# Performance work log

Hardware: AMD Instinct MI355X
Metric: run time of the kernel (lower is better)

Reference implementation:

```python
import jax, jax.numpy as jnp
import numpy as np

N_NODES = 50000


def _gcn_conv(x, edge_index, W, b):
    # x: [N, F_in], edge_index: [2, E] (with self-loops already added)
    n = x.shape[0]
    src, dst = edge_index[0], edge_index[1]
    h = x @ W  # [N, F_out] transform first (as in PyG GCNConv)
    deg = jax.ops.segment_sum(jnp.ones_like(dst, dtype=h.dtype), dst, num_segments=n)
    dinv = jax.lax.rsqrt(jnp.maximum(deg, 1.0))  # self-loops guarantee deg >= 1
    norm = dinv[src] * dinv[dst]  # [E]
    msg = h[src] * norm[:, None]  # [E, F_out] gather + scale
    out = jax.ops.segment_sum(msg, dst, num_segments=n)  # scatter-add to targets
    return out + b


def setup_inputs() -> dict:
    key = jax.random.key(0)
    k1, k2, k3, k4 = jax.random.split(key, 4)
    num_features, hidden, num_classes = 128, 128, 16
    n, e = N_NODES, 800000
    x = jax.random.normal(k1, (n, num_features), dtype=jnp.float32)
    edge_index = jax.random.randint(k2, (2, e), 0, n, dtype=jnp.int64)
    # add self-loops (PyG GCNConv default add_self_loops=True)
    loops = jnp.arange(n, dtype=jnp.int64)
    edge_index = jnp.concatenate([edge_index, jnp.stack([loops, loops])], axis=1)
    s1 = 1.0 / np.sqrt(num_features)
    s2 = 1.0 / np.sqrt(hidden)
    W1 = jax.random.uniform(k3, (num_features, hidden), jnp.float32, -s1, s1)
    b1 = jnp.zeros((hidden,), jnp.float32)
    W2 = jax.random.uniform(k4, (hidden, num_classes), jnp.float32, -s2, s2)
    b2 = jnp.zeros((num_classes,), jnp.float32)
    return {"x": x, "edge_index": edge_index, "W1": W1, "b1": b1, "W2": W2, "b2": b2}


def reference(x, edge_index, W1, b1, W2, b2):
    h = jax.nn.relu(_gcn_conv(x, edge_index, W1, b1))
    # dropout is identity in eval mode (deterministic reference)
    h = _gcn_conv(h, edge_index, W2, b2)
    return jax.nn.log_softmax(h, axis=1)
```

## Files before the change

kernel.cpp:

```cpp
#include <hip/hip_runtime.h>


typedef unsigned int uint32;
typedef unsigned short ushort16;
typedef __attribute__((ext_vector_type(8))) short bf16x8;
typedef __attribute__((ext_vector_type(4))) float f32x4;

#define NBMAX 1024
#define CHUNK 4096

__device__ inline unsigned short bf16rn(float f) {
    unsigned u = __float_as_uint(f);
    return (unsigned short)((u + 0x7fffu + ((u >> 16) & 1u)) >> 16);
}

__device__ inline void bffma(float2& a, float w, uint32 u) {
    a.x = fmaf(w, __uint_as_float(u << 16), a.x);
    a.y = fmaf(w, __uint_as_float(u & 0xffff0000u), a.y);
}


__global__ __launch_bounds__(256) void k_hist(const int* __restrict__ dst,
                                              int* __restrict__ bcnt,
                                              int E, int NB) {
    __shared__ int hl[NBMAX];
    int t = threadIdx.x;
    for (int i = t; i < NB; i += 256) hl[i] = 0;
    __syncthreads();
    int stride = gridDim.x * 256;
    for (int e = blockIdx.x * 256 + t; e < E; e += stride)
        atomicAdd(&hl[dst[e] >> 8], 1);
    __syncthreads();
    for (int i = t; i < NB; i += 256)
        if (hl[i]) atomicAdd(&bcnt[i], hl[i]);
}

__global__ __launch_bounds__(1024) void k_scanB(const int* __restrict__ bcnt,
                                                int* __restrict__ bbase,
                                                int* __restrict__ bfill,
                                                int NB, int E) {
    __shared__ int s[1024];
    int t = threadIdx.x;
    int v = (t < NB) ? bcnt[t] : 0;
    s[t] = v;
    __syncthreads();
    for (int off = 1; off < 1024; off <<= 1) {
        int u = (t >= off) ? s[t - off] : 0;
        __syncthreads();
        s[t] += u;
        __syncthreads();
    }
    if (t < NB) {
        bbase[t] = s[t] - v;
        bfill[t] = 0;
    }
    if (t == 0) bbase[NB] = E;
}

__global__ __launch_bounds__(256) void k_partition(const int* __restrict__ src,
                                                   const int* __restrict__ dst,
                                                   const int* __restrict__ bbase,
                                                   int* __restrict__ bfill,
                                                   int2* __restrict__ tmp,
                                                   int E, int NB) {
    __shared__ int cntL[NBMAX];
    __shared__ int baseL[NBMAX];
    int t = threadIdx.x;
    int e0 = blockIdx.x * CHUNK;
    int e1 = min(e0 + CHUNK, E);
    for (int i = t; i < NB; i += 256) cntL[i] = 0;
    __syncthreads();
    for (int e = e0 + t; e < e1; e += 256)
        atomicAdd(&cntL[dst[e] >> 8], 1);
    __syncthreads();
    for (int i = t; i < NB; i += 256) {
        int c = cntL[i];
        baseL[i] = c ? bbase[i] + atomicAdd(&bfill[i], c) : 0;
        cntL[i] = 0;
    }
    __syncthreads();
    for (int e = e0 + t; e < e1; e += 256) {
        int s = src[e], d = dst[e];
        int b = d >> 8;
        int r = atomicAdd(&cntL[b], 1);
        tmp[baseL[b] + r] = make_int2(s, d);
    }
}

__global__ __launch_bounds__(256) void k_bsort(const int2* __restrict__ tmp,
                                               const int* __restrict__ bbase,
                                               int* __restrict__ ssrc,
                                               int* __restrict__ rs,
                                               float* __restrict__ dinv,
                                               int N) {
    __shared__ int cnt[256];
    __shared__ int ofs[256];
    int t = threadIdx.x;
    int b = blockIdx.x;
    int base = bbase[b];
    int endb = bbase[b + 1];
    int node0 = b << 8;

    cnt[t] = 0;
    __syncthreads();
    for (int i = base + t; i < endb; i += 256)
        atomicAdd(&cnt[tmp[i].y & 255], 1);
    __syncthreads();

    int v = cnt[t];
    __syncthreads();
    for (int off = 1; off < 256; off <<= 1) {
        int u = (t >= off) ? cnt[t - off] : 0;
        __syncthreads();
        cnt[t] += u;
        __syncthreads();
    }
    int node = node0 + t;
    if (node < N) {
        dinv[node] = rsqrtf(fmaxf((float)v, 1.0f));
        rs[node] = base + cnt[t];
    }
    ofs[t] = base + cnt[t] - v;
    __syncthreads();

    for (int i = base + t; i < endb; i += 256) {
        int2 rec = tmp[i];
        int pos = atomicAdd(&ofs[rec.y & 255], 1);
        ssrc[pos] = rec.x;
    }
}


__global__ __launch_bounds__(256) void k_gemm1(const float* __restrict__ x,
                                               const float* __restrict__ W,
                                               ushort16* __restrict__ h, int N) {
    __shared__ unsigned short Wl[128 * 136];
    int t = threadIdx.x;
    const float4* Wg4 = (const float4*)W;
    for (int g = t; g < 128 * 32; g += 256) {
        int k = g >> 5, n4 = (g & 31) * 4;
        float4 v = Wg4[g];
        Wl[(n4 + 0) * 136 + k] = bf16rn(v.x);
        Wl[(n4 + 1) * 136 + k] = bf16rn(v.y);
        Wl[(n4 + 2) * 136 + k] = bf16rn(v.z);
        Wl[(n4 + 3) * 136 + k] = bf16rn(v.w);
    }
    __syncthreads();

    int wave = t >> 6, lane = t & 63;
    int quad = lane >> 4, ln = lane & 15;
    int rowbase = blockIdx.x * 64 + wave * 16;
    int arow = rowbase + ln;
    int rclamp = min(arow, N - 1);

    f32x4 acc[8];
    #pragma unroll
    for (int ct = 0; ct < 8; ++ct) acc[ct] = (f32x4){0.f, 0.f, 0.f, 0.f};

    #pragma unroll
    for (int q = 0; q < 4; ++q) {
        const float4* xr = (const float4*)(x + (size_t)rclamp * 128 + q * 32 + quad * 8);
        float4 a0 = xr[0], a1 = xr[1];
        bf16x8 afr;
        afr[0] = (short)bf16rn(a0.x); afr[1] = (short)bf16rn(a0.y);
        afr[2] = (short)bf16rn(a0.z); afr[3] = (short)bf16rn(a0.w);
        afr[4] = (short)bf16rn(a1.x); afr[5] = (short)bf16rn(a1.y);
        afr[6] = (short)bf16rn(a1.z); afr[7] = (short)bf16rn(a1.w);
        #pragma unroll
        for (int ct = 0; ct < 8; ++ct) {
            bf16x8 bfr = *(const bf16x8*)&Wl[(ct * 16 + ln) * 136 + q * 32 + quad * 8];
            acc[ct] = __builtin_amdgcn_mfma_f32_16x16x32_bf16(afr, bfr, acc[ct], 0, 0, 0);
        }
    }

    #pragma unroll
    for (int i = 0; i < 4; ++i) {
        int r = rowbase + quad * 4 + i;
        if (r < N) {
            ushort16* hp = h + (size_t)r * 128 + ln;
            #pragma unroll
            for (int ct = 0; ct < 8; ++ct)
                hp[ct * 16] = bf16rn(acc[ct][i]);
        }
    }
}

__global__ __launch_bounds__(256) void k_pull1(const int* __restrict__ rs,
                                               const int* __restrict__ ssrc,
                                               const float* __restrict__ dinv,
                                               const uint32* __restrict__ h,
                                               uint32* __restrict__ out1, int N) {
    int n = (blockIdx.x * 256 + threadIdx.x) >> 6;
    if (n >= N) return;
    int lane = threadIdx.x & 63;
    int start = __builtin_amdgcn_readfirstlane((n == 0) ? 0 : rs[n - 1]);
    int end   = __builtin_amdgcn_readfirstlane(rs[n]);
    float dn = dinv[n];
    float2 a0 = {0.f, 0.f}, a1 = {0.f, 0.f}, a2 = {0.f, 0.f}, a3 = {0.f, 0.f};
    int j = start;
    for (; j + 3 < end; j += 4) {
        int s0 = __builtin_amdgcn_readfirstlane(ssrc[j]);
        int s1 = __builtin_amdgcn_readfirstlane(ssrc[j + 1]);
        int s2 = __builtin_amdgcn_readfirstlane(ssrc[j + 2]);
        int s3 = __builtin_amdgcn_readfirstlane(ssrc[j + 3]);
        uint32 u0 = h[(size_t)s0 * 64 + lane];
        uint32 u1 = h[(size_t)s1 * 64 + lane];
        uint32 u2 = h[(size_t)s2 * 64 + lane];
        uint32 u3 = h[(size_t)s3 * 64 + lane];
        float w0 = dn * dinv[s0];
        float w1 = dn * dinv[s1];
        float w2 = dn * dinv[s2];
        float w3 = dn * dinv[s3];
        bffma(a0, w0, u0);
        bffma(a1, w1, u1);
        bffma(a2, w2, u2);
        bffma(a3, w3, u3);
    }
    for (; j < end; ++j) {
        int s0 = __builtin_amdgcn_readfirstlane(ssrc[j]);
        uint32 u0 = h[(size_t)s0 * 64 + lane];
        bffma(a0, dn * dinv[s0], u0);
    }
    float rx = (a0.x + a1.x) + (a2.x + a3.x);
    float ry = (a0.y + a1.y) + (a2.y + a3.y);
    out1[(size_t)n * 64 + lane] = ((uint32)bf16rn(ry) << 16) | bf16rn(rx);
}

__global__ __launch_bounds__(256) void k_gemm2(const uint32* __restrict__ out1,
                                               const float* __restrict__ b1,
                                               const float* __restrict__ W2,
                                               ushort16* __restrict__ h2, int N) {
    __shared__ float W2T[16 * 132];
    __shared__ float b1l[128];
    __shared__ float al[32 * 132];
    int t = threadIdx.x;
    int row0 = blockIdx.x * 32;

    for (int g = t; g < 2048; g += 256) {
        int k = g >> 4, f = g & 15;
        W2T[f * 132 + k] = W2[g];
    }
    if (t < 128) b1l[t] = b1[t];
    __syncthreads();

    float4* al4 = (float4*)al;
    const uint4* o4 = (const uint4*)out1;
    for (int g = t; g < 32 * 16; g += 256) {
        int r = g >> 4, k8 = g & 15;
        uint4 u = {0u, 0u, 0u, 0u};
        if (row0 + r < N) u = o4[(size_t)(row0 + r) * 16 + k8];
        const float* bb = &b1l[k8 * 8];
        float4 v0, v1;
        v0.x = fmaxf(__uint_as_float(u.x << 16)          + bb[0], 0.f);
        v0.y = fmaxf(__uint_as_float(u.x & 0xffff0000u)  + bb[1], 0.f);
        v0.z = fmaxf(__uint_as_float(u.y << 16)          + bb[2], 0.f);
        v0.w = fmaxf(__uint_as_float(u.y & 0xffff0000u)  + bb[3], 0.f);
        v1.x = fmaxf(__uint_as_float(u.z << 16)          + bb[4], 0.f);
        v1.y = fmaxf(__uint_as_float(u.z & 0xffff0000u)  + bb[5], 0.f);
        v1.z = fmaxf(__uint_as_float(u.w << 16)          + bb[6], 0.f);
        v1.w = fmaxf(__uint_as_float(u.w & 0xffff0000u)  + bb[7], 0.f);
        al4[r * 33 + k8 * 2]     = v0;
        al4[r * 33 + k8 * 2 + 1] = v1;
    }
    __syncthreads();

    int f = t & 15, r0 = t >> 4;
    const float4* W4 = (const float4*)W2T;
    float acc0 = 0.f, acc1 = 0.f;
    #pragma unroll 8
    for (int k4 = 0; k4 < 32; ++k4) {
        float4 w  = W4[f * 33 + k4];
        float4 x0 = al4[r0 * 33 + k4];
        float4 x1 = al4[(r0 + 16) * 33 + k4];
        acc0 = fmaf(x0.x, w.x, acc0); acc0 = fmaf(x0.y, w.y, acc0);
        acc0 = fmaf(x0.z, w.z, acc0); acc0 = fmaf(x0.w, w.w, acc0);
        acc1 = fmaf(x1.x, w.x, acc1); acc1 = fmaf(x1.y, w.y, acc1);
        acc1 = fmaf(x1.z, w.z, acc1); acc1 = fmaf(x1.w, w.w, acc1);
    }
    if (row0 + r0 < N)      h2[(size_t)(row0 + r0) * 16 + f] = bf16rn(acc0);
    if (row0 + r0 + 16 < N) h2[(size_t)(row0 + r0 + 16) * 16 + f] = bf16rn(acc1);
}

__global__ __launch_bounds__(256) void k_pull2(const int* __restrict__ rs,
                                               const int* __restrict__ ssrc,
                                               const float* __restrict__ dinv,
                                               const uint32* __restrict__ h2,
                                               const float* __restrict__ b2,
                                               float* __restrict__ out, int N) {
    int idx = blockIdx.x * 256 + threadIdx.x;
    int n = idx >> 3;
    if (n >= N) return;
    int c = idx & 7;
    int start = (n == 0) ? 0 : rs[n - 1];
    int end = rs[n];
    float dn = dinv[n];
    float acc0 = 0.f, acc1 = 0.f;
    for (int j = start; j < end; ++j) {
        int s = ssrc[j];
        float w = dn * dinv[s];
        uint32 u = h2[(size_t)s * 8 + c];
        acc0 = fmaf(w, __uint_as_float(u << 16), acc0);
        acc1 = fmaf(w, __uint_as_float(u & 0xffff0000u), acc1);
    }
    float v0 = acc0 + b2[2 * c];
    float v1 = acc1 + b2[2 * c + 1];
    float m = fmaxf(v0, v1);
    #pragma unroll
    for (int off = 1; off < 8; off <<= 1) m = fmaxf(m, __shfl_xor(m, off));
    float s = expf(v0 - m) + expf(v1 - m);
    #pragma unroll
    for (int off = 1; off < 8; off <<= 1) s += __shfl_xor(s, off);
    float ls = logf(s);
    float2 r = {v0 - m - ls, v1 - m - ls};
    ((float2*)out)[(size_t)n * 8 + c] = r;
}

extern "C" void kernel_launch(void* const* d_in, const int* in_sizes, int n_in,
                              void* d_out, int out_size, void* d_ws, size_t ws_size,
                              hipStream_t stream) {
    const float* x  = (const float*)d_in[0];
    const int*   ei = (const int*)d_in[1];
    const float* W1 = (const float*)d_in[2];
    const float* b1 = (const float*)d_in[3];
    const float* W2 = (const float*)d_in[4];
    const float* b2 = (const float*)d_in[5];
    float* out = (float*)d_out;

    const int E = in_sizes[1] / 2;
    const int N = in_sizes[0] / 128;
    const int NB = (N + 255) >> 8;
    const int* src  = ei;
    const int* dstv = ei + E;

    const int Npad = (N + 255) & ~255;
    const int Epad = (E + 255) & ~255;
    int*   bcnt  = (int*)d_ws;
    int*   bbase = bcnt + NBMAX;
    int*   bfill = bbase + NBMAX + 256;
    int*   rs    = bfill + NBMAX;
    float* dinv  = (float*)(rs + Npad);
    int2*  tmp   = (int2*)(dinv + Npad);
    int*   ssrc  = (int*)(tmp + Epad);
    ushort16* h  = (ushort16*)(ssrc + Epad);
    uint32* out1 = (uint32*)(h + (size_t)N * 128);
    ushort16* h2 = (ushort16*)h;

    hipMemsetAsync(bcnt, 0, NBMAX * sizeof(int), stream);
    k_hist<<<512, 256, 0, stream>>>(dstv, bcnt, E, NB);
    k_scanB<<<1, 1024, 0, stream>>>(bcnt, bbase, bfill, NB, E);
    k_partition<<<(E + CHUNK - 1) / CHUNK, 256, 0, stream>>>(src, dstv, bbase,
                                                             bfill, tmp, E, NB);
    k_bsort<<<NB, 256, 0, stream>>>(tmp, bbase, ssrc, rs, dinv, N);

    k_gemm1<<<(N + 63) / 64, 256, 0, stream>>>(x, W1, h, N);

    k_pull1<<<(N * 64 + 255) / 256, 256, 0, stream>>>(rs, ssrc, dinv,
                                                      (const uint32*)h, out1, N);

    k_gemm2<<<(N + 31) / 32, 256, 0, stream>>>(out1, b1, W2, h2, N);

    k_pull2<<<(N * 8 + 255) / 256, 256, 0, stream>>>(rs, ssrc, dinv,
                                                     (const uint32*)h2, b2, out, N);
}
```

Measured before the change: 202.8 us.

## Fuse all GCN stages into one cooperative persistent kernel with grid syncs

Merges histogram, scan, partition, bucket sort, both GEMMs and both aggregation passes into a single persistent kernel. The stages are separated by cooperative grid.sync calls, with a fallback that runs one phase per launch. The goal is to remove launch overhead and the memset between the nine launches. In exchange it risks lower occupancy with a capped grid, grid-sync cost, and idle blocks in the single-block scan phase. It also overlaps the sort-to-GEMM1 boundary with no sync, splits GEMM1 into two W halves to fit shared memory, and unrolls the pull1 loop to 8.

```diff
diff --git a/kernel.cpp b/kernel.cpp
--- a/kernel.cpp
+++ b/kernel.cpp
@@ -1,17 +1,21 @@
 #include <hip/hip_runtime.h>
+#include <hip/hip_cooperative_groups.h>
+
+namespace cg = cooperative_groups;
 
 
 typedef unsigned int uint32;
-typedef unsigned short ushort16;
+typedef unsigned short u16;
 typedef __attribute__((ext_vector_type(8))) short bf16x8;
 typedef __attribute__((ext_vector_type(4))) float f32x4;
 
 #define NBMAX 1024
 #define CHUNK 4096
-
-__device__ inline unsigned short bf16rn(float f) {
+#define SMEM_BYTES 25856
+
+__device__ inline u16 bf16rn(float f) {
     unsigned u = __float_as_uint(f);
-    return (unsigned short)((u + 0x7fffu + ((u >> 16) & 1u)) >> 16);
+    return (u16)((u + 0x7fffu + ((u >> 16) & 1u)) >> 16);
 }
 
 __device__ inline void bffma(float2& a, float w, uint32 u) {
@@ -19,300 +23,324 @@
     a.y = fmaf(w, __uint_as_float(u & 0xffff0000u), a.y);
 }
 
-
-__global__ __launch_bounds__(256) void k_hist(const int* __restrict__ dst,
-                                              int* __restrict__ bcnt,
-                                              int E, int NB) {
-    __shared__ int hl[NBMAX];
-    int t = threadIdx.x;
-    for (int i = t; i < NB; i += 256) hl[i] = 0;
-    __syncthreads();
-    int stride = gridDim.x * 256;
-    for (int e = blockIdx.x * 256 + t; e < E; e += stride)
-        atomicAdd(&hl[dst[e] >> 8], 1);
-    __syncthreads();
-    for (int i = t; i < NB; i += 256)
-        if (hl[i]) atomicAdd(&bcnt[i], hl[i]);
-}
-
-__global__ __launch_bounds__(1024) void k_scanB(const int* __restrict__ bcnt,
-                                                int* __restrict__ bbase,
-                                                int* __restrict__ bfill,
-                                                int NB, int E) {
-    __shared__ int s[1024];
-    int t = threadIdx.x;
-    int v = (t < NB) ? bcnt[t] : 0;
-    s[t] = v;
-    __syncthreads();
-    for (int off = 1; off < 1024; off <<= 1) {
-        int u = (t >= off) ? s[t - off] : 0;
-        __syncthreads();
-        s[t] += u;
-        __syncthreads();
-    }
-    if (t < NB) {
-        bbase[t] = s[t] - v;
-        bfill[t] = 0;
-    }
-    if (t == 0) bbase[NB] = E;
-}
-
-__global__ __launch_bounds__(256) void k_partition(const int* __restrict__ src,
-                                                   const int* __restrict__ dst,
-                                                   const int* __restrict__ bbase,
-                                                   int* __restrict__ bfill,
-                                                   int2* __restrict__ tmp,
-                                                   int E, int NB) {
-    __shared__ int cntL[NBMAX];
-    __shared__ int baseL[NBMAX];
-    int t = threadIdx.x;
-    int e0 = blockIdx.x * CHUNK;
-    int e1 = min(e0 + CHUNK, E);
-    for (int i = t; i < NB; i += 256) cntL[i] = 0;
-    __syncthreads();
-    for (int e = e0 + t; e < e1; e += 256)
-        atomicAdd(&cntL[dst[e] >> 8], 1);
-    __syncthreads();
-    for (int i = t; i < NB; i += 256) {
-        int c = cntL[i];
-        baseL[i] = c ? bbase[i] + atomicAdd(&bfill[i], c) : 0;
-        cntL[i] = 0;
-    }
-    __syncthreads();
-    for (int e = e0 + t; e < e1; e += 256) {
-        int s = src[e], d = dst[e];
-        int b = d >> 8;
-        int r = atomicAdd(&cntL[b], 1);
-        tmp[baseL[b] + r] = make_int2(s, d);
-    }
-}
-
-__global__ __launch_bounds__(256) void k_bsort(const int2* __restrict__ tmp,
-                                               const int* __restrict__ bbase,
-                                               int* __restrict__ ssrc,
-                                               int* __restrict__ rs,
-                                               float* __restrict__ dinv,
-                                               int N) {
-    __shared__ int cnt[256];
-    __shared__ int ofs[256];
-    int t = threadIdx.x;
-    int b = blockIdx.x;
-    int base = bbase[b];
-    int endb = bbase[b + 1];
-    int node0 = b << 8;
-
-    cnt[t] = 0;
-    __syncthreads();
-    for (int i = base + t; i < endb; i += 256)
-        atomicAdd(&cnt[tmp[i].y & 255], 1);
-    __syncthreads();
-
-    int v = cnt[t];
-    __syncthreads();
-    for (int off = 1; off < 256; off <<= 1) {
-        int u = (t >= off) ? cnt[t - off] : 0;
-        __syncthreads();
-        cnt[t] += u;
-        __syncthreads();
-    }
-    int node = node0 + t;
-    if (node < N) {
-        dinv[node] = rsqrtf(fmaxf((float)v, 1.0f));
-        rs[node] = base + cnt[t];
-    }
-    ofs[t] = base + cnt[t] - v;
-    __syncthreads();
-
-    for (int i = base + t; i < endb; i += 256) {
-        int2 rec = tmp[i];
-        int pos = atomicAdd(&ofs[rec.y & 255], 1);
-        ssrc[pos] = rec.x;
-    }
-}
-
-
-__global__ __launch_bounds__(256) void k_gemm1(const float* __restrict__ x,
-                                               const float* __restrict__ W,
-                                               ushort16* __restrict__ h, int N) {
-    __shared__ unsigned short Wl[128 * 136];
-    int t = threadIdx.x;
-    const float4* Wg4 = (const float4*)W;
-    for (int g = t; g < 128 * 32; g += 256) {
-        int k = g >> 5, n4 = (g & 31) * 4;
-        float4 v = Wg4[g];
-        Wl[(n4 + 0) * 136 + k] = bf16rn(v.x);
-        Wl[(n4 + 1) * 136 + k] = bf16rn(v.y);
-        Wl[(n4 + 2) * 136 + k] = bf16rn(v.z);
-        Wl[(n4 + 3) * 136 + k] = bf16rn(v.w);
-    }
-    __syncthreads();
-
-    int wave = t >> 6, lane = t & 63;
-    int quad = lane >> 4, ln = lane & 15;
-    int rowbase = blockIdx.x * 64 + wave * 16;
-    int arow = rowbase + ln;
-    int rclamp = min(arow, N - 1);
-
-    f32x4 acc[8];
-    #pragma unroll
-    for (int ct = 0; ct < 8; ++ct) acc[ct] = (f32x4){0.f, 0.f, 0.f, 0.f};
-
-    #pragma unroll
-    for (int q = 0; q < 4; ++q) {
-        const float4* xr = (const float4*)(x + (size_t)rclamp * 128 + q * 32 + quad * 8);
-        float4 a0 = xr[0], a1 = xr[1];
-        bf16x8 afr;
-        afr[0] = (short)bf16rn(a0.x); afr[1] = (short)bf16rn(a0.y);
-        afr[2] = (short)bf16rn(a0.z); afr[3] = (short)bf16rn(a0.w);
-        afr[4] = (short)bf16rn(a1.x); afr[5] = (short)bf16rn(a1.y);
-        afr[6] = (short)bf16rn(a1.z); afr[7] = (short)bf16rn(a1.w);
+__global__ __launch_bounds__(256, 2) void k_mega(
+    const float* __restrict__ x, const int* __restrict__ src,
+    const int* __restrict__ dstv,
+    const float* __restrict__ W1, const float* __restrict__ b1,
+    const float* __restrict__ W2, const float* __restrict__ b2,
+    int* __restrict__ bcnt, int* __restrict__ bbase, int* __restrict__ bfill,
+    int* __restrict__ rs, float* __restrict__ dinv,
+    int2* __restrict__ tmp, int* __restrict__ ssrc,
+    u16* __restrict__ h, uint32* __restrict__ out1,
+    float* __restrict__ outp, int N, int E, int NB, int p0, int p1)
+{
+    __shared__ __align__(16) unsigned char smem[SMEM_BYTES];
+    const int t = threadIdx.x;
+    const int nbk = gridDim.x;
+    const int gtid = blockIdx.x * 256 + t;
+    const int gsz = nbk * 256;
+
+    cg::grid_group grid = cg::this_grid();
+    #define INPH(p) (p0 <= (p) && (p) <= p1)
+    #define GSYNC(p) if (p0 < (p) && (p) <= p1) grid.sync()
+
+    if (INPH(0)) {
+        for (int i = gtid; i < NBMAX; i += gsz) bcnt[i] = 0;
+    }
+    GSYNC(1);
+
+    if (INPH(1)) {
+        int* hl = (int*)smem;
+        for (int i = t; i < NB; i += 256) hl[i] = 0;
+        __syncthreads();
+        for (int e = gtid; e < E; e += gsz) atomicAdd(&hl[dstv[e] >> 8], 1);
+        __syncthreads();
+        for (int i = t; i < NB; i += 256)
+            if (hl[i]) atomicAdd(&bcnt[i], hl[i]);
+        __syncthreads();
+    }
+    GSYNC(2);
+
+    if (INPH(2) && blockIdx.x == 0) {
+        int* s = (int*)smem;
+        int v[4];
+        int sum = 0;
         #pragma unroll
-        for (int ct = 0; ct < 8; ++ct) {
-            bf16x8 bfr = *(const bf16x8*)&Wl[(ct * 16 + ln) * 136 + q * 32 + quad * 8];
-            acc[ct] = __builtin_amdgcn_mfma_f32_16x16x32_bf16(afr, bfr, acc[ct], 0, 0, 0);
-        }
-    }
-
-    #pragma unroll
-    for (int i = 0; i < 4; ++i) {
-        int r = rowbase + quad * 4 + i;
-        if (r < N) {
-            ushort16* hp = h + (size_t)r * 128 + ln;
+        for (int i = 0; i < 4; ++i) {
+            int idx = t * 4 + i;
+            v[i] = (idx < NB) ? bcnt[idx] : 0;
+            sum += v[i];
+        }
+        s[t] = sum;
+        __syncthreads();
+        for (int off = 1; off < 256; off <<= 1) {
+            int u = (t >= off) ? s[t - off] : 0;
+            __syncthreads();
+            s[t] += u;
+            __syncthreads();
+        }
+        int excl = (t > 0) ? s[t - 1] : 0;
+        #pragma unroll
+        for (int i = 0; i < 4; ++i) {
+            int idx = t * 4 + i;
+            if (idx < NB) { bbase[idx] = excl; bfill[idx] = 0; }
+            excl += v[i];
+        }
+        if (t == 0) bbase[NB] = E;
+        __syncthreads();
+    }
+    GSYNC(3);
+
+    if (INPH(3)) {
+        int* cntL = (int*)smem;
+        int* baseL = cntL + NBMAX;
+        int nchunk = (E + CHUNK - 1) / CHUNK;
+        for (int c = blockIdx.x; c < nchunk; c += nbk) {
+            int e0 = c * CHUNK, e1 = min(e0 + CHUNK, E);
+            for (int i = t; i < NB; i += 256) cntL[i] = 0;
+            __syncthreads();
+            for (int e = e0 + t; e < e1; e += 256)
+                atomicAdd(&cntL[dstv[e] >> 8], 1);
+            __syncthreads();
+            for (int i = t; i < NB; i += 256) {
+                int cc = cntL[i];
+                baseL[i] = cc ? bbase[i] + atomicAdd(&bfill[i], cc) : 0;
+                cntL[i] = 0;
+            }
+            __syncthreads();
+            for (int e = e0 + t; e < e1; e += 256) {
+                int sv = src[e], d = dstv[e];
+                int b = d >> 8;
+                int r = atomicAdd(&cntL[b], 1);
+                tmp[baseL[b] + r] = make_int2(sv, d);
+            }
+            __syncthreads();
+        }
+    }
+    GSYNC(4);
+
+    if (INPH(4)) {
+        int* cnt = (int*)smem;
+        int* ofs = cnt + 256;
+        for (int b = blockIdx.x; b < NB; b += nbk) {
+            int base = bbase[b];
+            int endb = bbase[b + 1];
+            int node0 = b << 8;
+            cnt[t] = 0;
+            __syncthreads();
+            for (int i = base + t; i < endb; i += 256)
+                atomicAdd(&cnt[tmp[i].y & 255], 1);
+            __syncthreads();
+            int v = cnt[t];
+            __syncthreads();
+            for (int off = 1; off < 256; off <<= 1) {
+                int u = (t >= off) ? cnt[t - off] : 0;
+                __syncthreads();
+                cnt[t] += u;
+                __syncthreads();
+            }
+            int node = node0 + t;
+            if (node < N) {
+                dinv[node] = rsqrtf(fmaxf((float)v, 1.0f));
+                rs[node] = base + cnt[t];
+            }
+            ofs[t] = base + cnt[t] - v;
+            __syncthreads();
+            for (int i = base + t; i < endb; i += 256) {
+                int2 rec = tmp[i];
+                int pos = atomicAdd(&ofs[rec.y & 255], 1);
+                ssrc[pos] = rec.x;
+            }
+            __syncthreads();
+        }
+    }
+
+    if (INPH(5)) {
+        u16* Wl = (u16*)smem;
+        int wave = t >> 6, lane = t & 63;
+        int quad = lane >> 4, ln = lane & 15;
+        int ntile = (N + 63) / 64;
+        const float4* Wg4 = (const float4*)W1;
+        for (int half = 0; half < 2; ++half) {
+            __syncthreads();
+            for (int g = t; g < 64 * 32; g += 256) {
+                int k = g >> 4, nq = g & 15;
+                float4 v = Wg4[k * 32 + half * 16 + nq];
+                int n4 = nq * 4;
+                Wl[(n4 + 0) * 136 + k] = bf16rn(v.x);
+                Wl[(n4 + 1) * 136 + k] = bf16rn(v.y);
+                Wl[(n4 + 2) * 136 + k] = bf16rn(v.z);
+                Wl[(n4 + 3) * 136 + k] = bf16rn(v.w);
+            }
+            __syncthreads();
+            for (int tile = blockIdx.x; tile < ntile; tile += nbk) {
+                int rowbase = tile * 64 + wave * 16;
+                int rclamp = min(rowbase + ln, N - 1);
+                f32x4 acc[4];
+                #pragma unroll
+                for (int ct = 0; ct < 4; ++ct) acc[ct] = (f32x4){0.f, 0.f, 0.f, 0.f};
+                #pragma unroll
+                for (int q = 0; q < 4; ++q) {
+                    const float4* xr =
+                        (const float4*)(x + (size_t)rclamp * 128 + q * 32 + quad * 8);
+                    float4 a0 = xr[0], a1 = xr[1];
+                    bf16x8 afr;
+                    afr[0] = (short)bf16rn(a0.x); afr[1] = (short)bf16rn(a0.y);
+                    afr[2] = (short)bf16rn(a0.z); afr[3] = (short)bf16rn(a0.w);
+                    afr[4] = (short)bf16rn(a1.x); afr[5] = (short)bf16rn(a1.y);
+                    afr[6] = (short)bf16rn(a1.z); afr[7] = (short)bf16rn(a1.w);
+                    #pragma unroll
+                    for (int ct = 0; ct < 4; ++ct) {
+                        bf16x8 bfr =
+                            *(const bf16x8*)&Wl[(ct * 16 + ln) * 136 + q * 32 + quad * 8];
+                        acc[ct] = __builtin_amdgcn_mfma_f32_16x16x32_bf16(
+                            afr, bfr, acc[ct], 0, 0, 0);
+                    }
+                }
+                #pragma unroll
+                for (int i = 0; i < 4; ++i) {
+                    int r = rowbase + quad * 4 + i;
+                    if (r < N) {
+                        u16* hp = h + (size_t)r * 128 + half * 64 + ln;
+                        #pragma unroll
+                        for (int ct = 0; ct < 4; ++ct)
+                            hp[ct * 16] = bf16rn(acc[ct][i]);
+                    }
+                }
+            }
+        }
+    }
+    GSYNC(6);
+
+    if (INPH(6)) {
+        int wave = t >> 6, lane = t & 63;
+        const uint32* hu = (const uint32*)h;
+        int ngrp = (N + 3) >> 2;
+        for (int g = blockIdx.x; g < ngrp; g += nbk) {
+            int n = g * 4 + wave;
+            if (n >= N) continue;
+            int start = __builtin_amdgcn_readfirstlane((n == 0) ? 0 : rs[n - 1]);
+            int end   = __builtin_amdgcn_readfirstlane(rs[n]);
+            float dn = dinv[n];
+            float2 a[8];
             #pragma unroll
-            for (int ct = 0; ct < 8; ++ct)
-                hp[ct * 16] = bf16rn(acc[ct][i]);
-        }
-    }
-}
-
-__global__ __launch_bounds__(256) void k_pull1(const int* __restrict__ rs,
-                                               const int* __restrict__ ssrc,
-                                               const float* __restrict__ dinv,
-                                               const uint32* __restrict__ h,
-                                               uint32* __restrict__ out1, int N) {
-    int n = (blockIdx.x * 256 + threadIdx.x) >> 6;
-    if (n >= N) return;
-    int lane = threadIdx.x & 63;
-    int start = __builtin_amdgcn_readfirstlane((n == 0) ? 0 : rs[n - 1]);
-    int end   = __builtin_amdgcn_readfirstlane(rs[n]);
-    float dn = dinv[n];
-    float2 a0 = {0.f, 0.f}, a1 = {0.f, 0.f}, a2 = {0.f, 0.f}, a3 = {0.f, 0.f};
-    int j = start;
-    for (; j + 3 < end; j += 4) {
-        int s0 = __builtin_amdgcn_readfirstlane(ssrc[j]);
-        int s1 = __builtin_amdgcn_readfirstlane(ssrc[j + 1]);
-        int s2 = __builtin_amdgcn_readfirstlane(ssrc[j + 2]);
-        int s3 = __builtin_amdgcn_readfirstlane(ssrc[j + 3]);
-        uint32 u0 = h[(size_t)s0 * 64 + lane];
-        uint32 u1 = h[(size_t)s1 * 64 + lane];
-        uint32 u2 = h[(size_t)s2 * 64 + lane];
-        uint32 u3 = h[(size_t)s3 * 64 + lane];
-        float w0 = dn * dinv[s0];
-        float w1 = dn * dinv[s1];
-        float w2 = dn * dinv[s2];
-        float w3 = dn * dinv[s3];
-        bffma(a0, w0, u0);
-        bffma(a1, w1, u1);
-        bffma(a2, w2, u2);
-        bffma(a3, w3, u3);
-    }
-    for (; j < end; ++j) {
-        int s0 = __builtin_amdgcn_readfirstlane(ssrc[j]);
-        uint32 u0 = h[(size_t)s0 * 64 + lane];
-        bffma(a0, dn * dinv[s0], u0);
-    }
-    float rx = (a0.x + a1.x) + (a2.x + a3.x);
-    float ry = (a0.y + a1.y) + (a2.y + a3.y);
-    out1[(size_t)n * 64 + lane] = ((uint32)bf16rn(ry) << 16) | bf16rn(rx);
-}
-
-__global__ __launch_bounds__(256) void k_gemm2(const uint32* __restrict__ out1,
-                                               const float* __restrict__ b1,
-                                               const float* __restrict__ W2,
-                                               ushort16* __restrict__ h2, int N) {
-    __shared__ float W2T[16 * 132];
-    __shared__ float b1l[128];
-    __shared__ float al[32 * 132];
-    int t = threadIdx.x;
-    int row0 = blockIdx.x * 32;
-
-    for (int g = t; g < 2048; g += 256) {
-        int k = g >> 4, f = g & 15;
-        W2T[f * 132 + k] = W2[g];
-    }
-    if (t < 128) b1l[t] = b1[t];
-    __syncthreads();
-
-    float4* al4 = (float4*)al;
-    const uint4* o4 = (const uint4*)out1;
-    for (int g = t; g < 32 * 16; g += 256) {
-        int r = g >> 4, k8 = g & 15;
-        uint4 u = {0u, 0u, 0u, 0u};
-        if (row0 + r < N) u = o4[(size_t)(row0 + r) * 16 + k8];
-        const float* bb = &b1l[k8 * 8];
-        float4 v0, v1;
-        v0.x = fmaxf(__uint_as_float(u.x << 16)          + bb[0], 0.f);
-        v0.y = fmaxf(__uint_as_float(u.x & 0xffff0000u)  + bb[1], 0.f);
-        v0.z = fmaxf(__uint_as_float(u.y << 16)          + bb[2], 0.f);
-        v0.w = fmaxf(__uint_as_float(u.y & 0xffff0000u)  + bb[3], 0.f);
-        v1.x = fmaxf(__uint_as_float(u.z << 16)          + bb[4], 0.f);
-        v1.y = fmaxf(__uint_as_float(u.z & 0xffff0000u)  + bb[5], 0.f);
-        v1.z = fmaxf(__uint_as_float(u.w << 16)          + bb[6], 0.f);
-        v1.w = fmaxf(__uint_as_float(u.w & 0xffff0000u)  + bb[7], 0.f);
-        al4[r * 33 + k8 * 2]     = v0;
-        al4[r * 33 + k8 * 2 + 1] = v1;
-    }
-    __syncthreads();
-
-    int f = t & 15, r0 = t >> 4;
-    const float4* W4 = (const float4*)W2T;
-    float acc0 = 0.f, acc1 = 0.f;
-    #pragma unroll 8
-    for (int k4 = 0; k4 < 32; ++k4) {
-        float4 w  = W4[f * 33 + k4];
-        float4 x0 = al4[r0 * 33 + k4];
-        float4 x1 = al4[(r0 + 16) * 33 + k4];
-        acc0 = fmaf(x0.x, w.x, acc0); acc0 = fmaf(x0.y, w.y, acc0);
-        acc0 = fmaf(x0.z, w.z, acc0); acc0 = fmaf(x0.w, w.w, acc0);
-        acc1 = fmaf(x1.x, w.x, acc1); acc1 = fmaf(x1.y, w.y, acc1);
-        acc1 = fmaf(x1.z, w.z, acc1); acc1 = fmaf(x1.w, w.w, acc1);
-    }
-    if (row0 + r0 < N)      h2[(size_t)(row0 + r0) * 16 + f] = bf16rn(acc0);
-    if (row0 + r0 + 16 < N) h2[(size_t)(row0 + r0 + 16) * 16 + f] = bf16rn(acc1);
-}
-
-__global__ __launch_bounds__(256) void k_pull2(const int* __restrict__ rs,
-                                               const int* __restrict__ ssrc,
-                                               const float* __restrict__ dinv,
-                                               const uint32* __restrict__ h2,
-                                               const float* __restrict__ b2,
-                                               float* __restrict__ out, int N) {
-    int idx = blockIdx.x * 256 + threadIdx.x;
-    int n = idx >> 3;
-    if (n >= N) return;
-    int c = idx & 7;
-    int start = (n == 0) ? 0 : rs[n - 1];
-    int end = rs[n];
-    float dn = dinv[n];
-    float acc0 = 0.f, acc1 = 0.f;
-    for (int j = start; j < end; ++j) {
-        int s = ssrc[j];
-        float w = dn * dinv[s];
-        uint32 u = h2[(size_t)s * 8 + c];
-        acc0 = fmaf(w, __uint_as_float(u << 16), acc0);
-        acc1 = fmaf(w, __uint_as_float(u & 0xffff0000u), acc1);
-    }
-    float v0 = acc0 + b2[2 * c];
-    float v1 = acc1 + b2[2 * c + 1];
-    float m = fmaxf(v0, v1);
-    #pragma unroll
-    for (int off = 1; off < 8; off <<= 1) m = fmaxf(m, __shfl_xor(m, off));
-    float s = expf(v0 - m) + expf(v1 - m);
-    #pragma unroll
-    for (int off = 1; off < 8; off <<= 1) s += __shfl_xor(s, off);
-    float ls = logf(s);
-    float2 r = {v0 - m - ls, v1 - m - ls};
-    ((float2*)out)[(size_t)n * 8 + c] = r;
+            for (int i = 0; i < 8; ++i) a[i] = (float2){0.f, 0.f};
+            int j = start;
+            for (; j + 7 < end; j += 8) {
+                int si[8];
+                uint32 u[8];
+                float w[8];
+                #pragma unroll
+                for (int i = 0; i < 8; ++i)
+                    si[i] = __builtin_amdgcn_readfirstlane(ssrc[j + i]);
+                #pragma unroll
+                for (int i = 0; i < 8; ++i)
+                    u[i] = hu[(size_t)si[i] * 64 + lane];
+                #pragma unroll
+                for (int i = 0; i < 8; ++i)
+                    w[i] = dn * dinv[si[i]];
+                #pragma unroll
+                for (int i = 0; i < 8; ++i)
+                    bffma(a[i], w[i], u[i]);
+            }
+            for (; j < end; ++j) {
+                int s0 = __builtin_amdgcn_readfirstlane(ssrc[j]);
+                bffma(a[0], dn * dinv[s0], hu[(size_t)s0 * 64 + lane]);
+            }
+            float rx = ((a[0].x + a[1].x) + (a[2].x + a[3].x)) +
+                       ((a[4].x + a[5].x) + (a[6].x + a[7].x));
+            float ry = ((a[0].y + a[1].y) + (a[2].y + a[3].y)) +
+                       ((a[4].y + a[5].y) + (a[6].y + a[7].y));
+            out1[(size_t)n * 64 + lane] = ((uint32)bf16rn(ry) << 16) | bf16rn(rx);
+        }
+    }
+    GSYNC(7);
+
+    if (INPH(7)) {
+        float* W2T = (float*)smem;
+        float* b1l = W2T + 16 * 132;
+        float4* al4 = (float4*)(b1l + 128);
+        u16* h2 = h;
+        for (int g = t; g < 2048; g += 256) {
+            int k = g >> 4, f = g & 15;
+            W2T[f * 132 + k] = W2[g];
+        }
+        if (t < 128) b1l[t] = b1[t];
+        __syncthreads();
+
+        int f = t & 15, r0 = t >> 4;
+        const float4* W4 = (const float4*)W2T;
+        const uint4* o4 = (const uint4*)out1;
+        int ntile = (N + 31) / 32;
+        for (int tile = blockIdx.x; tile < ntile; tile += nbk) {
+            int row0 = tile * 32;
+            for (int g = t; g < 32 * 16; g += 256) {
+                int r = g >> 4, k8 = g & 15;
+                uint4 u = {0u, 0u, 0u, 0u};
+                if (row0 + r < N) u = o4[(size_t)(row0 + r) * 16 + k8];
+                const float* bb = &b1l[k8 * 8];
+                float4 v0, v1;
+                v0.x = fmaxf(__uint_as_float(u.x << 16)         + bb[0], 0.f);
+                v0.y = fmaxf(__uint_as_float(u.x & 0xffff0000u) + bb[1], 0.f);
+                v0.z = fmaxf(__uint_as_float(u.y << 16)         + bb[2], 0.f);
+                v0.w = fmaxf(__uint_as_float(u.y & 0xffff0000u) + bb[3], 0.f);
+                v1.x = fmaxf(__uint_as_float(u.z << 16)         + bb[4], 0.f);
+                v1.y = fmaxf(__uint_as_float(u.z & 0xffff0000u) + bb[5], 0.f);
+                v1.z = fmaxf(__uint_as_float(u.w << 16)         + bb[6], 0.f);
+                v1.w = fmaxf(__uint_as_float(u.w & 0xffff0000u) + bb[7], 0.f);
+                al4[r * 33 + k8 * 2]     = v0;
+                al4[r * 33 + k8 * 2 + 1] = v1;
+            }
+            __syncthreads();
+            float acc0 = 0.f, acc1 = 0.f;
+            #pragma unroll 8
+            for (int k4 = 0; k4 < 32; ++k4) {
+                float4 w  = W4[f * 33 + k4];
+                float4 x0 = al4[r0 * 33 + k4];
+                float4 x1 = al4[(r0 + 16) * 33 + k4];
+                acc0 = fmaf(x0.x, w.x, acc0); acc0 = fmaf(x0.y, w.y, acc0);
+                acc0 = fmaf(x0.z, w.z, acc0); acc0 = fmaf(x0.w, w.w, acc0);
+                acc1 = fmaf(x1.x, w.x, acc1); acc1 = fmaf(x1.y, w.y, acc1);
+                acc1 = fmaf(x1.z, w.z, acc1); acc1 = fmaf(x1.w, w.w, acc1);
+            }
+            if (row0 + r0 < N)      h2[(size_t)(row0 + r0) * 16 + f] = bf16rn(acc0);
+            if (row0 + r0 + 16 < N) h2[(size_t)(row0 + r0 + 16) * 16 + f] = bf16rn(acc1);
+            __syncthreads();
+        }
+    }
+    GSYNC(8);
+
+    if (INPH(8)) {
+        const uint32* h2u = (const uint32*)h;
+        for (int idx = gtid; idx < N * 8; idx += gsz) {
+            int n = idx >> 3;
+            int c = idx & 7;
+            int start = (n == 0) ? 0 : rs[n - 1];
+            int end = rs[n];
+            float dn = dinv[n];
+            float acc0 = 0.f, acc1 = 0.f;
+            for (int j = start; j < end; ++j) {
+                int s = ssrc[j];
+                float w = dn * dinv[s];
+                uint32 u = h2u[(size_t)s * 8 + c];
+                acc0 = fmaf(w, __uint_as_float(u << 16), acc0);
+                acc1 = fmaf(w, __uint_as_float(u & 0xffff0000u), acc1);
+            }
+            float v0 = acc0 + b2[2 * c];
+            float v1 = acc1 + b2[2 * c + 1];
+            float m = fmaxf(v0, v1);
+            #pragma unroll
+            for (int off = 1; off < 8; off <<= 1) m = fmaxf(m, __shfl_xor(m, off));
+            float s = expf(v0 - m) + expf(v1 - m);
+            #pragma unroll
+            for (int off = 1; off < 8; off <<= 1) s += __shfl_xor(s, off);
+            float ls = logf(s);
+            float2 r = {v0 - m - ls, v1 - m - ls};
+            ((float2*)outp)[(size_t)n * 8 + c] = r;
+        }
+    }
+    #undef INPH
+    #undef GSYNC
 }
 
 extern "C" void kernel_launch(void* const* d_in, const int* in_sizes, int n_in,
@@ -324,7 +352,7 @@
     const float* b1 = (const float*)d_in[3];
     const float* W2 = (const float*)d_in[4];
     const float* b2 = (const float*)d_in[5];
-    float* out = (float*)d_out;
+    float* outp = (float*)d_out;
 
     const int E = in_sizes[1] / 2;
     const int N = in_sizes[0] / 128;
@@ -341,24 +369,46 @@
     float* dinv  = (float*)(rs + Npad);
     int2*  tmp   = (int2*)(dinv + Npad);
     int*   ssrc  = (int*)(tmp + Epad);
-    ushort16* h  = (ushort16*)(ssrc + Epad);
+    u16*   h     = (u16*)(ssrc + Epad);
     uint32* out1 = (uint32*)(h + (size_t)N * 128);
-    ushort16* h2 = (ushort16*)h;
-
-    hipMemsetAsync(bcnt, 0, NBMAX * sizeof(int), stream);
-    k_hist<<<512, 256, 0, stream>>>(dstv, bcnt, E, NB);
-    k_scanB<<<1, 1024, 0, stream>>>(bcnt, bbase, bfill, NB, E);
-    k_partition<<<(E + CHUNK - 1) / CHUNK, 256, 0, stream>>>(src, dstv, bbase,
-                                                             bfill, tmp, E, NB);
-    k_bsort<<<NB, 256, 0, stream>>>(tmp, bbase, ssrc, rs, dinv, N);
-
-    k_gemm1<<<(N + 63) / 64, 256, 0, stream>>>(x, W1, h, N);
-
-    k_pull1<<<(N * 64 + 255) / 256, 256, 0, stream>>>(rs, ssrc, dinv,
-                                                      (const uint32*)h, out1, N);
-
-    k_gemm2<<<(N + 31) / 32, 256, 0, stream>>>(out1, b1, W2, h2, N);
-
-    k_pull2<<<(N * 8 + 255) / 256, 256, 0, stream>>>(rs, ssrc, dinv,
-                                                     (const uint32*)h2, b2, out, N);
+
+    int dev = 0;
+    hipGetDevice(&dev);
+    int coop = 0;
+    hipDeviceGetAttribute(&coop, hipDeviceAttributeCooperativeLaunch, dev);
+    int numCU = 0;
+    hipDeviceGetAttribute(&numCU, hipDeviceAttributeMultiprocessorCount, dev);
+    int maxB = 0;
+    hipOccupancyMaxActiveBlocksPerMultiprocessor(&maxB, k_mega, 256, 0);
+
+    if (coop && maxB >= 1 && numCU >= 1) {
+        int gridB = maxB * numCU;
+        if (gridB > 2048) gridB = 2048;
+        int p0 = 0, p1 = 8;
+        void* args[] = {
+            (void*)&x, (void*)&src, (void*)&dstv,
+            (void*)&W1, (void*)&b1, (void*)&W2, (void*)&b2,
+            (void*)&bcnt, (void*)&bbase, (void*)&bfill,
+            (void*)&rs, (void*)&dinv, (void*)&tmp, (void*)&ssrc,
+            (void*)&h, (void*)&out1, (void*)&outp,
+            (void*)&N, (void*)&E, (void*)&NB, (void*)&p0, (void*)&p1,
+        };
+        hipLaunchCooperativeKernel((const void*)k_mega, dim3(gridB), dim3(256),
+                                   args, 0, stream);
+    } else {
+        const int nchunk = (E + CHUNK - 1) / CHUNK;
+        #define LP(ph, g) k_mega<<<(g), 256, 0, stream>>>( \
+            x, src, dstv, W1, b1, W2, b2, bcnt, bbase, bfill, rs, dinv, tmp, \
+            ssrc, h, out1, outp, N, E, NB, (ph), (ph))
+        LP(0, 64);
+        LP(1, 512);
+        LP(2, 1);
+        LP(3, nchunk);
+        LP(4, NB);
+        LP(5, (N + 63) / 64);
+        LP(6, (N + 3) / 4);
+        LP(7, (N + 31) / 32);
+        LP(8, (N * 8 + 255) / 256);
+        #undef LP
+    }
 }
```

Result: slower. 535.6 us (+164.1%).

## Fuse destination histogram into GEMM1 launch and deepen pull1 gather unroll

Applied to the files above, without the earlier changes.

Merges the dst-bucket histogram and the first GEMM into one launch, with extra blocks doing the histogram into per-block partial arrays instead of global atomics. This removes the memset and a separate launch and lets the histogram overlap with the MFMA work. k_scanB now sums the partials itself. The layer-1 pull loop is unrolled from 4 to 8 edges with 8 accumulators to keep more gathers in flight, at the cost of more registers. The partials buffer holds 128 blocks, which caps E at about 1M edges.

```diff
diff --git a/kernel.cpp b/kernel.cpp
--- a/kernel.cpp
+++ b/kernel.cpp
@@ -2,16 +2,17 @@
 
 
 typedef unsigned int uint32;
-typedef unsigned short ushort16;
+typedef unsigned short u16;
 typedef __attribute__((ext_vector_type(8))) short bf16x8;
 typedef __attribute__((ext_vector_type(4))) float f32x4;
 
 #define NBMAX 1024
 #define CHUNK 4096
-
-__device__ inline unsigned short bf16rn(float f) {
+#define EH 8192
+
+__device__ inline u16 bf16rn(float f) {
     unsigned u = __float_as_uint(f);
-    return (unsigned short)((u + 0x7fffu + ((u >> 16) & 1u)) >> 16);
+    return (u16)((u + 0x7fffu + ((u >> 16) & 1u)) >> 16);
 }
 
 __device__ inline void bffma(float2& a, float w, uint32 u) {
@@ -19,124 +20,30 @@
     a.y = fmaf(w, __uint_as_float(u & 0xffff0000u), a.y);
 }
 
-
-__global__ __launch_bounds__(256) void k_hist(const int* __restrict__ dst,
-                                              int* __restrict__ bcnt,
-                                              int E, int NB) {
-    __shared__ int hl[NBMAX];
-    int t = threadIdx.x;
-    for (int i = t; i < NB; i += 256) hl[i] = 0;
-    __syncthreads();
-    int stride = gridDim.x * 256;
-    for (int e = blockIdx.x * 256 + t; e < E; e += stride)
-        atomicAdd(&hl[dst[e] >> 8], 1);
-    __syncthreads();
-    for (int i = t; i < NB; i += 256)
-        if (hl[i]) atomicAdd(&bcnt[i], hl[i]);
-}
-
-__global__ __launch_bounds__(1024) void k_scanB(const int* __restrict__ bcnt,
-                                                int* __restrict__ bbase,
-                                                int* __restrict__ bfill,
-                                                int NB, int E) {
-    __shared__ int s[1024];
-    int t = threadIdx.x;
-    int v = (t < NB) ? bcnt[t] : 0;
-    s[t] = v;
-    __syncthreads();
-    for (int off = 1; off < 1024; off <<= 1) {
-        int u = (t >= off) ? s[t - off] : 0;
-        __syncthreads();
-        s[t] += u;
-        __syncthreads();
-    }
-    if (t < NB) {
-        bbase[t] = s[t] - v;
-        bfill[t] = 0;
-    }
-    if (t == 0) bbase[NB] = E;
-}
-
-__global__ __launch_bounds__(256) void k_partition(const int* __restrict__ src,
-                                                   const int* __restrict__ dst,
-                                                   const int* __restrict__ bbase,
-                                                   int* __restrict__ bfill,
-                                                   int2* __restrict__ tmp,
-                                                   int E, int NB) {
-    __shared__ int cntL[NBMAX];
-    __shared__ int baseL[NBMAX];
-    int t = threadIdx.x;
-    int e0 = blockIdx.x * CHUNK;
-    int e1 = min(e0 + CHUNK, E);
-    for (int i = t; i < NB; i += 256) cntL[i] = 0;
-    __syncthreads();
-    for (int e = e0 + t; e < e1; e += 256)
-        atomicAdd(&cntL[dst[e] >> 8], 1);
-    __syncthreads();
-    for (int i = t; i < NB; i += 256) {
-        int c = cntL[i];
-        baseL[i] = c ? bbase[i] + atomicAdd(&bfill[i], c) : 0;
-        cntL[i] = 0;
-    }
-    __syncthreads();
-    for (int e = e0 + t; e < e1; e += 256) {
-        int s = src[e], d = dst[e];
-        int b = d >> 8;
-        int r = atomicAdd(&cntL[b], 1);
-        tmp[baseL[b] + r] = make_int2(s, d);
-    }
-}
-
-__global__ __launch_bounds__(256) void k_bsort(const int2* __restrict__ tmp,
-                                               const int* __restrict__ bbase,
-                                               int* __restrict__ ssrc,
-                                               int* __restrict__ rs,
-                                               float* __restrict__ dinv,
-                                               int N) {
-    __shared__ int cnt[256];
-    __shared__ int ofs[256];
-    int t = threadIdx.x;
-    int b = blockIdx.x;
-    int base = bbase[b];
-    int endb = bbase[b + 1];
-    int node0 = b << 8;
-
-    cnt[t] = 0;
-    __syncthreads();
-    for (int i = base + t; i < endb; i += 256)
-        atomicAdd(&cnt[tmp[i].y & 255], 1);
-    __syncthreads();
-
-    int v = cnt[t];
-    __syncthreads();
-    for (int off = 1; off < 256; off <<= 1) {
-        int u = (t >= off) ? cnt[t - off] : 0;
-        __syncthreads();
-        cnt[t] += u;
-        __syncthreads();
-    }
-    int node = node0 + t;
-    if (node < N) {
-        dinv[node] = rsqrtf(fmaxf((float)v, 1.0f));
-        rs[node] = base + cnt[t];
-    }
-    ofs[t] = base + cnt[t] - v;
-    __syncthreads();
-
-    for (int i = base + t; i < endb; i += 256) {
-        int2 rec = tmp[i];
-        int pos = atomicAdd(&ofs[rec.y & 255], 1);
-        ssrc[pos] = rec.x;
-    }
-}
-
-
-__global__ __launch_bounds__(256) void k_gemm1(const float* __restrict__ x,
-                                               const float* __restrict__ W,
-                                               ushort16* __restrict__ h, int N) {
-    __shared__ unsigned short Wl[128 * 136];
-    int t = threadIdx.x;
-    const float4* Wg4 = (const float4*)W;
+__global__ __launch_bounds__(256) void k_combo(
+    const float* __restrict__ x, const float* __restrict__ W1,
+    const int* __restrict__ dstv, int* __restrict__ partials,
+    u16* __restrict__ h, int N, int E, int NB, int ntile)
+{
+    __shared__ __align__(16) unsigned char smem[128 * 136 * 2];
+    int t = threadIdx.x;
+
+    if ((int)blockIdx.x >= ntile) {
+        int* hl = (int*)smem;
+        int hb = blockIdx.x - ntile;
+        int e0 = hb * EH, e1 = min(e0 + EH, E);
+        for (int i = t; i < NB; i += 256) hl[i] = 0;
+        __syncthreads();
+        for (int e = e0 + t; e < e1; e += 256)
+            atomicAdd(&hl[dstv[e] >> 8], 1);
+        __syncthreads();
+        int* pr = partials + (size_t)hb * NBMAX;
+        for (int i = t; i < NB; i += 256) pr[i] = hl[i];
+        return;
+    }
+
+    u16* Wl = (u16*)smem;
+    const float4* Wg4 = (const float4*)W1;
     for (int g = t; g < 128 * 32; g += 256) {
         int k = g >> 5, n4 = (g & 31) * 4;
         float4 v = Wg4[g];
@@ -150,8 +57,7 @@
     int wave = t >> 6, lane = t & 63;
     int quad = lane >> 4, ln = lane & 15;
     int rowbase = blockIdx.x * 64 + wave * 16;
-    int arow = rowbase + ln;
-    int rclamp = min(arow, N - 1);
+    int rclamp = min(rowbase + ln, N - 1);
 
     f32x4 acc[8];
     #pragma unroll
@@ -172,12 +78,11 @@
             acc[ct] = __builtin_amdgcn_mfma_f32_16x16x32_bf16(afr, bfr, acc[ct], 0, 0, 0);
         }
     }
-
     #pragma unroll
     for (int i = 0; i < 4; ++i) {
         int r = rowbase + quad * 4 + i;
         if (r < N) {
-            ushort16* hp = h + (size_t)r * 128 + ln;
+            u16* hp = h + (size_t)r * 128 + ln;
             #pragma unroll
             for (int ct = 0; ct < 8; ++ct)
                 hp[ct * 16] = bf16rn(acc[ct][i]);
@@ -185,51 +90,146 @@
     }
 }
 
-__global__ __launch_bounds__(256) void k_pull1(const int* __restrict__ rs,
-                                               const int* __restrict__ ssrc,
-                                               const float* __restrict__ dinv,
-                                               const uint32* __restrict__ h,
-                                               uint32* __restrict__ out1, int N) {
+__global__ __launch_bounds__(1024) void k_scanB(
+    const int* __restrict__ partials, int* __restrict__ bbase,
+    int* __restrict__ bfill, int NB, int E, int NH)
+{
+    __shared__ int s[1024];
+    int t = threadIdx.x;
+    int v = 0;
+    if (t < NB)
+        for (int p = 0; p < NH; ++p) v += partials[(size_t)p * NBMAX + t];
+    s[t] = v;
+    __syncthreads();
+    for (int off = 1; off < 1024; off <<= 1) {
+        int u = (t >= off) ? s[t - off] : 0;
+        __syncthreads();
+        s[t] += u;
+        __syncthreads();
+    }
+    if (t < NB) {
+        bbase[t] = s[t] - v;
+        bfill[t] = 0;
+    }
+    if (t == 0) bbase[NB] = E;
+}
+
+__global__ __launch_bounds__(256) void k_partition(
+    const int* __restrict__ src, const int* __restrict__ dstv,
+    const int* __restrict__ bbase, int* __restrict__ bfill,
+    int2* __restrict__ tmp, int E, int NB)
+{
+    __shared__ int cntL[NBMAX];
+    __shared__ int baseL[NBMAX];
+    int t = threadIdx.x;
+    int e0 = blockIdx.x * CHUNK;
+    int e1 = min(e0 + CHUNK, E);
+    for (int i = t; i < NB; i += 256) cntL[i] = 0;
+    __syncthreads();
+    for (int e = e0 + t; e < e1; e += 256)
+        atomicAdd(&cntL[dstv[e] >> 8], 1);
+    __syncthreads();
+    for (int i = t; i < NB; i += 256) {
+        int cc = cntL[i];
+        baseL[i] = cc ? bbase[i] + atomicAdd(&bfill[i], cc) : 0;
+        cntL[i] = 0;
+    }
+    __syncthreads();
+    for (int e = e0 + t; e < e1; e += 256) {
+        int sv = src[e], d = dstv[e];
+        int b = d >> 8;
+        int r = atomicAdd(&cntL[b], 1);
+        tmp[baseL[b] + r] = make_int2(sv, d);
+    }
+}
+
+__global__ __launch_bounds__(256) void k_bsort(
+    const int2* __restrict__ tmp, const int* __restrict__ bbase,
+    int* __restrict__ ssrc, int* __restrict__ rs,
+    float* __restrict__ dinv, int N)
+{
+    __shared__ int cnt[256];
+    __shared__ int ofs[256];
+    int t = threadIdx.x;
+    int b = blockIdx.x;
+    int base = bbase[b];
+    int endb = bbase[b + 1];
+    int node0 = b << 8;
+
+    cnt[t] = 0;
+    __syncthreads();
+    for (int i = base + t; i < endb; i += 256)
+        atomicAdd(&cnt[tmp[i].y & 255], 1);
+    __syncthreads();
+    int v = cnt[t];
+    __syncthreads();
+    for (int off = 1; off < 256; off <<= 1) {
+        int u = (t >= off) ? cnt[t - off] : 0;
+        __syncthreads();
+        cnt[t] += u;
+        __syncthreads();
+    }
+    int node = node0 + t;
+    if (node < N) {
+        dinv[node] = rsqrtf(fmaxf((float)v, 1.0f));
+        rs[node] = base + cnt[t];
+    }
+    ofs[t] = base + cnt[t] - v;
+    __syncthreads();
+    for (int i = base + t; i < endb; i += 256) {
+        int2 rec = tmp[i];
+        int pos = atomicAdd(&ofs[rec.y & 255], 1);
+        ssrc[pos] = rec.x;
+    }
+}
+
+__global__ __launch_bounds__(256) void k_pull1(
+    const int* __restrict__ rs, const int* __restrict__ ssrc,
+    const float* __restrict__ dinv, const uint32* __restrict__ h,
+    uint32* __restrict__ out1, int N)
+{
     int n = (blockIdx.x * 256 + threadIdx.x) >> 6;
     if (n >= N) return;
     int lane = threadIdx.x & 63;
     int start = __builtin_amdgcn_readfirstlane((n == 0) ? 0 : rs[n - 1]);
     int end   = __builtin_amdgcn_readfirstlane(rs[n]);
     float dn = dinv[n];
-    float2 a0 = {0.f, 0.f}, a1 = {0.f, 0.f}, a2 = {0.f, 0.f}, a3 = {0.f, 0.f};
+    float2 a[8];
+    #pragma unroll
+    for (int i = 0; i < 8; ++i) a[i] = (float2){0.f, 0.f};
     int j = start;
-    for (; j + 3 < end; j += 4) {
-        int s0 = __builtin_amdgcn_readfirstlane(ssrc[j]);
-        int s1 = __builtin_amdgcn_readfirstlane(ssrc[j + 1]);
-        int s2 = __builtin_amdgcn_readfirstlane(ssrc[j + 2]);
-        int s3 = __builtin_amdgcn_readfirstlane(ssrc[j + 3]);
-        uint32 u0 = h[(size_t)s0 * 64 + lane];
-        uint32 u1 = h[(size_t)s1 * 64 + lane];
-        uint32 u2 = h[(size_t)s2 * 64 + lane];
-        uint32 u3 = h[(size_t)s3 * 64 + lane];
-        float w0 = dn * dinv[s0];
-        float w1 = dn * dinv[s1];
-        float w2 = dn * dinv[s2];
-        float w3 = dn * dinv[s3];
-        bffma(a0, w0, u0);
-        bffma(a1, w1, u1);
-        bffma(a2, w2, u2);
-        bffma(a3, w3, u3);
+    for (; j + 7 < end; j += 8) {
+        int si[8];
+        uint32 u[8];
+        float w[8];
+        #pragma unroll
+        for (int i = 0; i < 8; ++i)
+            si[i] = __builtin_amdgcn_readfirstlane(ssrc[j + i]);
+        #pragma unroll
+        for (int i = 0; i < 8; ++i)
+            u[i] = h[(size_t)si[i] * 64 + lane];
+        #pragma unroll
+        for (int i = 0; i < 8; ++i)
+            w[i] = dn * dinv[si[i]];
+        #pragma unroll
+        for (int i = 0; i < 8; ++i)
+            bffma(a[i], w[i], u[i]);
     }
     for (; j < end; ++j) {
         int s0 = __builtin_amdgcn_readfirstlane(ssrc[j]);
-        uint32 u0 = h[(size_t)s0 * 64 + lane];
-        bffma(a0, dn * dinv[s0], u0);
-    }
-    float rx = (a0.x + a1.x) + (a2.x + a3.x);
-    float ry = (a0.y + a1.y) + (a2.y + a3.y);
+        bffma(a[0], dn * dinv[s0], h[(size_t)s0 * 64 + lane]);
+    }
+    float rx = ((a[0].x + a[1].x) + (a[2].x + a[3].x)) +
+               ((a[4].x + a[5].x) + (a[6].x + a[7].x));
+    float ry = ((a[0].y + a[1].y) + (a[2].y + a[3].y)) +
+               ((a[4].y + a[5].y) + (a[6].y + a[7].y));
     out1[(size_t)n * 64 + lane] = ((uint32)bf16rn(ry) << 16) | bf16rn(rx);
 }
 
-__global__ __launch_bounds__(256) void k_gemm2(const uint32* __restrict__ out1,
-                                               const float* __restrict__ b1,
-                                               const float* __restrict__ W2,
-                                               ushort16* __restrict__ h2, int N) {
+__global__ __launch_bounds__(256) void k_gemm2(
+    const uint32* __restrict__ out1, const float* __restrict__ b1,
+    const float* __restrict__ W2, u16* __restrict__ h2, int N)
+{
     __shared__ float W2T[16 * 132];
     __shared__ float b1l[128];
     __shared__ float al[32 * 132];
@@ -251,14 +251,14 @@
         if (row0 + r < N) u = o4[(size_t)(row0 + r) * 16 + k8];
         const float* bb = &b1l[k8 * 8];
         float4 v0, v1;
-        v0.x = fmaxf(__uint_as_float(u.x << 16)          + bb[0], 0.f);
-        v0.y = fmaxf(__uint_as_float(u.x & 0xffff0000u)  + bb[1], 0.f);
-        v0.z = fmaxf(__uint_as_float(u.y << 16)          + bb[2], 0.f);
-        v0.w = fmaxf(__uint_as_float(u.y & 0xffff0000u)  + bb[3], 0.f);
-        v1.x = fmaxf(__uint_as_float(u.z << 16)          + bb[4], 0.f);
-        v1.y = fmaxf(__uint_as_float(u.z & 0xffff0000u)  + bb[5], 0.f);
-        v1.z = fmaxf(__uint_as_float(u.w << 16)          + bb[6], 0.f);
-        v1.w = fmaxf(__uint_as_float(u.w & 0xffff0000u)  + bb[7], 0.f);
+        v0.x = fmaxf(__uint_as_float(u.x << 16)         + bb[0], 0.f);
+        v0.y = fmaxf(__uint_as_float(u.x & 0xffff0000u) + bb[1], 0.f);
+        v0.z = fmaxf(__uint_as_float(u.y << 16)         + bb[2], 0.f);
+        v0.w = fmaxf(__uint_as_float(u.y & 0xffff0000u) + bb[3], 0.f);
+        v1.x = fmaxf(__uint_as_float(u.z << 16)         + bb[4], 0.f);
+        v1.y = fmaxf(__uint_as_float(u.z & 0xffff0000u) + bb[5], 0.f);
+        v1.z = fmaxf(__uint_as_float(u.w << 16)         + bb[6], 0.f);
+        v1.w = fmaxf(__uint_as_float(u.w & 0xffff0000u) + bb[7], 0.f);
         al4[r * 33 + k8 * 2]     = v0;
         al4[r * 33 + k8 * 2 + 1] = v1;
     }
@@ -281,12 +281,11 @@
     if (row0 + r0 + 16 < N) h2[(size_t)(row0 + r0 + 16) * 16 + f] = bf16rn(acc1);
 }
 
-__global__ __launch_bounds__(256) void k_pull2(const int* __restrict__ rs,
-                                               const int* __restrict__ ssrc,
-                                               const float* __restrict__ dinv,
-                                               const uint32* __restrict__ h2,
-                                               const float* __restrict__ b2,
-                                               float* __restrict__ out, int N) {
+__global__ __launch_bounds__(256) void k_pull2(
+    const int* __restrict__ rs, const int* __restrict__ ssrc,
+    const float* __restrict__ dinv, const uint32* __restrict__ h2,
+    const float* __restrict__ b2, float* __restrict__ out, int N)
+{
     int idx = blockIdx.x * 256 + threadIdx.x;
     int n = idx >> 3;
     if (n >= N) return;
@@ -324,41 +323,37 @@
     const float* b1 = (const float*)d_in[3];
     const float* W2 = (const float*)d_in[4];
     const float* b2 = (const float*)d_in[5];
-    float* out = (float*)d_out;
+    float* outp = (float*)d_out;
 
     const int E = in_sizes[1] / 2;
     const int N = in_sizes[0] / 128;
     const int NB = (N + 255) >> 8;
+    const int NH = (E + EH - 1) / EH;
+    const int ntile = (N + 63) / 64;
     const int* src  = ei;
     const int* dstv = ei + E;
 
     const int Npad = (N + 255) & ~255;
     const int Epad = (E + 255) & ~255;
-    int*   bcnt  = (int*)d_ws;
-    int*   bbase = bcnt + NBMAX;
+    int*   partials = (int*)d_ws;
+    int*   bbase = partials + 128 * NBMAX;
     int*   bfill = bbase + NBMAX + 256;
     int*   rs    = bfill + NBMAX;
     float* dinv  = (float*)(rs + Npad);
     int2*  tmp   = (int2*)(dinv + Npad);
     int*   ssrc  = (int*)(tmp + Epad);
-    ushort16* h  = (ushort16*)(ssrc + Epad);
+    u16*   h     = (u16*)(ssrc + Epad);
     uint32* out1 = (uint32*)(h + (size_t)N * 128);
-    ushort16* h2 = (ushort16*)h;
-
-    hipMemsetAsync(bcnt, 0, NBMAX * sizeof(int), stream);
-    k_hist<<<512, 256, 0, stream>>>(dstv, bcnt, E, NB);
-    k_scanB<<<1, 1024, 0, stream>>>(bcnt, bbase, bfill, NB, E);
+    u16*   h2    = h;
+
+    k_combo<<<ntile + NH, 256, 0, stream>>>(x, W1, dstv, partials, h, N, E, NB, ntile);
+    k_scanB<<<1, 1024, 0, stream>>>(partials, bbase, bfill, NB, E, NH);
     k_partition<<<(E + CHUNK - 1) / CHUNK, 256, 0, stream>>>(src, dstv, bbase,
                                                              bfill, tmp, E, NB);
     k_bsort<<<NB, 256, 0, stream>>>(tmp, bbase, ssrc, rs, dinv, N);
-
-    k_gemm1<<<(N + 63) / 64, 256, 0, stream>>>(x, W1, h, N);
-
     k_pull1<<<(N * 64 + 255) / 256, 256, 0, stream>>>(rs, ssrc, dinv,
                                                       (const uint32*)h, out1, N);
-
     k_gemm2<<<(N + 31) / 32, 256, 0, stream>>>(out1, b1, W2, h2, N);
-
     k_pull2<<<(N * 8 + 255) / 256, 256, 0, stream>>>(rs, ssrc, dinv,
-                                                     (const uint32*)h2, b2, out, N);
-}
+                                                     (const uint32*)h2, b2, outp, N);
+}
```

Result: no change. 200.1 us (-1.4%).
